# Kernel tuning notes

Hardware: AMD Instinct MI355X
Metric: run time of the kernel (lower is better)

## Reference

```python
import jax, jax.numpy as jnp
import numpy as np

D_MODEL = 1024
N_HEADS = 16
D_K = D_MODEL // N_HEADS
B, S = 4, 2048


def setup_inputs() -> dict:
    key = jax.random.key(0)
    ks = jax.random.split(key, 11)
    scale = 1.0 / np.sqrt(D_MODEL)
    inp = {
        "q": jax.random.normal(ks[0], (B, S, D_MODEL), dtype=jnp.float32),
        "k": jax.random.normal(ks[1], (B, S, D_MODEL), dtype=jnp.float32),
        "v": jax.random.normal(ks[2], (B, S, D_MODEL), dtype=jnp.float32),
        "Wq": jax.random.normal(ks[3], (D_MODEL, D_MODEL), dtype=jnp.float32) * scale,
        "bq": jnp.zeros((D_MODEL,), dtype=jnp.float32),
        "Wk": jax.random.normal(ks[4], (D_MODEL, D_MODEL), dtype=jnp.float32) * scale,
        "bk": jnp.zeros((D_MODEL,), dtype=jnp.float32),
        "Wv": jax.random.normal(ks[5], (D_MODEL, D_MODEL), dtype=jnp.float32) * scale,
        "bv": jnp.zeros((D_MODEL,), dtype=jnp.float32),
        "Wo": jax.random.normal(ks[6], (D_MODEL, D_MODEL), dtype=jnp.float32) * scale,
        "bo": jnp.zeros((D_MODEL,), dtype=jnp.float32),
    }
    return inp


def _split_heads(x):
    # [B, S, D] -> [B, H, S, d_k]
    b, s, _ = x.shape
    return x.reshape(b, s, N_HEADS, D_K).transpose(0, 2, 1, 3)


def reference(q, k, v, Wq, bq, Wk, bk, Wv, bv, Wo, bo):
    Q = _split_heads(q @ Wq.T + bq)  # [B, H, S, d_k]
    K = _split_heads(k @ Wk.T + bk)
    V = _split_heads(v @ Wv.T + bv)
    scale = 1.0 / jnp.sqrt(jnp.asarray(D_K, Q.dtype))
    scores = jnp.einsum("bhqd,bhkd->bhqk", Q, K) * scale  # [B, H, S, S]
    attn = jax.nn.softmax(scores, axis=-1)
    out = jnp.einsum("bhqk,bhkd->bhqd", attn, V)  # [B, H, S, d_k]
    out = out.transpose(0, 2, 1, 3).reshape(q.shape[0], q.shape[1], D_MODEL)
    return out @ Wo.T + bo
```

## Files before the change

### kernel.cpp

```cpp
#include <hip/hip_runtime.h>


typedef __bf16 bf16;
typedef bf16 bf16x4 __attribute__((ext_vector_type(4)));
typedef bf16 bf16x8 __attribute__((ext_vector_type(8)));
typedef float f32x4 __attribute__((ext_vector_type(4)));

__device__ __forceinline__ void gld_lds16(const void* g, void* l) {
  __builtin_amdgcn_global_load_lds((__attribute__((address_space(1))) void*)g,
                                   (__attribute__((address_space(3))) void*)l,
                                   16, 0, 0);
}

__global__ __launch_bounds__(256) void cvt3(const float* __restrict__ a,
                                            const float* __restrict__ b,
                                            const float* __restrict__ c,
                                            bf16* __restrict__ oa,
                                            bf16* __restrict__ ob,
                                            bf16* __restrict__ oc) {
  const int z = blockIdx.y;
  const float* s = (z == 0) ? a : (z == 1) ? b : c;
  bf16* d = (z == 0) ? oa : (z == 1) ? ob : oc;
  const int i = blockIdx.x * 256 + threadIdx.x;
  float4 f = reinterpret_cast<const float4*>(s)[i];
  bf16x4 o = {(bf16)f.x, (bf16)f.y, (bf16)f.z, (bf16)f.w};
  reinterpret_cast<bf16x4*>(d)[i] = o;
}

__global__ __launch_bounds__(256) void cvt4(const float* __restrict__ a,
                                            const float* __restrict__ b,
                                            const float* __restrict__ c,
                                            const float* __restrict__ dd,
                                            bf16* __restrict__ oa,
                                            bf16* __restrict__ ob,
                                            bf16* __restrict__ oc,
                                            bf16* __restrict__ od) {
  const int z = blockIdx.y;
  const float* s = (z == 0) ? a : (z == 1) ? b : (z == 2) ? c : dd;
  bf16* d = (z == 0) ? oa : (z == 1) ? ob : (z == 2) ? oc : od;
  const int i = blockIdx.x * 256 + threadIdx.x;
  float4 f = reinterpret_cast<const float4*>(s)[i];
  bf16x4 o = {(bf16)f.x, (bf16)f.y, (bf16)f.z, (bf16)f.w};
  reinterpret_cast<bf16x4*>(d)[i] = o;
}

__device__ __forceinline__ void gemm_core(const bf16* __restrict__ A,
                                          const bf16* __restrict__ B,
                                          bf16* As, bf16* Bs, int t,
                                          int m0, int n0, f32x4 acc[4][4]) {
  constexpr int K = 1024;
  const int lane = t & 63;
  const int wave = t >> 6;
  const int wm = wave >> 1, wn = wave & 1;
  const int r16 = lane & 15, quad = lane >> 4;

  for (int k0 = 0; k0 < K; k0 += 32) {
    __syncthreads();
#pragma unroll
    for (int hh = 0; hh < 2; ++hh) {
      const int c = t + hh * 256;
      const int row = c >> 2, kk = (c & 3) * 8;
      gld_lds16(A + (size_t)(m0 + row) * K + k0 + kk, As + c * 8);
      gld_lds16(B + (size_t)(n0 + row) * K + k0 + kk, Bs + c * 8);
    }
    __syncthreads();
    bf16x8 af[4], bfr[4];
#pragma unroll
    for (int i = 0; i < 4; ++i)
      af[i] = *(const bf16x8*)&As[(wm * 64 + i * 16 + r16) * 32 + quad * 8];
#pragma unroll
    for (int i = 0; i < 4; ++i)
      bfr[i] = *(const bf16x8*)&Bs[(wn * 64 + i * 16 + r16) * 32 + quad * 8];
#pragma unroll
    for (int mi = 0; mi < 4; ++mi)
#pragma unroll
      for (int ni = 0; ni < 4; ++ni)
        acc[mi][ni] = __builtin_amdgcn_mfma_f32_16x16x32_bf16(af[mi], bfr[ni],
                                                              acc[mi][ni], 0, 0, 0);
  }
}

__global__ __launch_bounds__(256) void gemm_qkv(
    const bf16* __restrict__ qb, const bf16* __restrict__ kb,
    const bf16* __restrict__ vb, const bf16* __restrict__ Wqb,
    const bf16* __restrict__ Wkb, const bf16* __restrict__ Wvb,
    const float* __restrict__ bq, const float* __restrict__ bk,
    const float* __restrict__ bv, bf16* __restrict__ Qp,
    bf16* __restrict__ Kp, bf16* __restrict__ VTt, float qscale) {
  __shared__ alignas(16) bf16 As[128 * 32];
  __shared__ alignas(16) bf16 Bs[128 * 32];
  const int which = blockIdx.z;
  const bf16* A = (which == 0) ? qb : (which == 1) ? kb : vb;
  const bf16* W = (which == 0) ? Wqb : (which == 1) ? Wkb : Wvb;
  const float* bias = (which == 0) ? bq : (which == 1) ? bk : bv;
  const float oscale = (which == 0) ? qscale : 1.0f;
  bf16* Cb = (which == 0) ? Qp : (which == 1) ? Kp : VTt;

  const int t = threadIdx.x;
  const int m0 = blockIdx.y * 128, n0 = blockIdx.x * 128;
  f32x4 acc[4][4] = {};
  gemm_core(A, W, As, Bs, t, m0, n0, acc);

  const int lane = t & 63, wave = t >> 6;
  const int wm = wave >> 1, wn = wave & 1;
  const int r16 = lane & 15, quad = lane >> 4;
#pragma unroll
  for (int mi = 0; mi < 4; ++mi) {
    const int m = m0 + wm * 64 + mi * 16 + quad * 4;
#pragma unroll
    for (int ni = 0; ni < 4; ++ni) {
      const int n = n0 + wn * 64 + ni * 16 + r16;
      const float bv_ = bias[n];
      const int h = n >> 6, dh = n & 63;
      if (which < 2) {
#pragma unroll
        for (int i = 0; i < 4; ++i) {
          const int mm = m + i;
          const int b = mm >> 11, s = mm & 2047;
          Cb[(((size_t)(b * 16 + h)) * 2048 + s) * 64 + dh] =
              (bf16)((acc[mi][ni][i] + bv_) * oscale);
        }
      } else {
        const int b = m >> 11, s = m & 2047;
        bf16x4 pk;
#pragma unroll
        for (int i = 0; i < 4; ++i) pk[i] = (bf16)(acc[mi][ni][i] + bv_);
        *(bf16x4*)&Cb[(((size_t)(b * 16 + h)) * 64 + dh) * 2048 + s] = pk;
      }
    }
  }
}

__global__ __launch_bounds__(256) void gemm_out(const bf16* __restrict__ A,
                                                const bf16* __restrict__ W,
                                                const float* __restrict__ bias,
                                                float* __restrict__ Cf) {
  __shared__ alignas(16) bf16 As[128 * 32];
  __shared__ alignas(16) bf16 Bs[128 * 32];
  const int t = threadIdx.x;
  const int m0 = blockIdx.y * 128, n0 = blockIdx.x * 128;
  f32x4 acc[4][4] = {};
  gemm_core(A, W, As, Bs, t, m0, n0, acc);

  const int lane = t & 63, wave = t >> 6;
  const int wm = wave >> 1, wn = wave & 1;
  const int r16 = lane & 15, quad = lane >> 4;
#pragma unroll
  for (int mi = 0; mi < 4; ++mi) {
    const int m = m0 + wm * 64 + mi * 16 + quad * 4;
#pragma unroll
    for (int ni = 0; ni < 4; ++ni) {
      const int n = n0 + wn * 64 + ni * 16 + r16;
      const float bv_ = bias[n];
#pragma unroll
      for (int i = 0; i < 4; ++i)
        Cf[(size_t)(m + i) * 1024 + n] = acc[mi][ni][i] + bv_;
    }
  }
}

__global__ __launch_bounds__(256) void attn_fwd(const bf16* __restrict__ Qp,
                                                const bf16* __restrict__ Kp,
                                                const bf16* __restrict__ VT,
                                                bf16* __restrict__ AO) {
  __shared__ alignas(16) bf16 Ks[64 * 72];
  __shared__ alignas(16) bf16 Vs[64 * 72];
  __shared__ alignas(16) bf16 Ps[128 * 72];
  __shared__ float Lr[128];
  const int t = threadIdx.x, lane = t & 63, wave = t >> 6;
  const int r16 = lane & 15, quad = lane >> 4;
  const int bh = blockIdx.y;
  const int q0 = blockIdx.x * 128;
  const int qw = wave * 32;
  const bf16* Qb = Qp + (size_t)bh * (2048 * 64);
  const bf16* Kb = Kp + (size_t)bh * (2048 * 64);
  const bf16* Vb = VT + (size_t)bh * (64 * 2048);

  bf16x8 qf[2][2];
#pragma unroll
  for (int nq = 0; nq < 2; ++nq)
#pragma unroll
    for (int ks = 0; ks < 2; ++ks)
      qf[nq][ks] = *(const bf16x8*)&Qb[(size_t)(q0 + qw + nq * 16 + r16) * 64 +
                                       ks * 32 + quad * 8];

  const int c0 = t * 2, c1 = t * 2 + 1;
  const int kr0 = c0 >> 3, kc0 = (c0 & 7) * 8;
  const int kr1 = c1 >> 3, kc1 = (c1 & 7) * 8;

  bf16x8 kreg0 = *(const bf16x8*)(Kb + (size_t)kr0 * 64 + kc0);
  bf16x8 kreg1 = *(const bf16x8*)(Kb + (size_t)kr1 * 64 + kc1);
  bf16x8 vreg0 = *(const bf16x8*)(Vb + (size_t)kr0 * 2048 + kc0);
  bf16x8 vreg1 = *(const bf16x8*)(Vb + (size_t)kr1 * 2048 + kc1);

  f32x4 o[2][4] = {};
  float lrow[2] = {0.f, 0.f};

  for (int kv0 = 0; kv0 < 2048; kv0 += 64) {
    __syncthreads();
    *(bf16x8*)&Ks[kr0 * 72 + kc0] = kreg0;
    *(bf16x8*)&Ks[kr1 * 72 + kc1] = kreg1;
    *(bf16x8*)&Vs[kr0 * 72 + kc0] = vreg0;
    *(bf16x8*)&Vs[kr1 * 72 + kc1] = vreg1;
    __syncthreads();

    if (kv0 + 64 < 2048) {
      const int nx = kv0 + 64;
      kreg0 = *(const bf16x8*)(Kb + (size_t)(nx + kr0) * 64 + kc0);
      kreg1 = *(const bf16x8*)(Kb + (size_t)(nx + kr1) * 64 + kc1);
      vreg0 = *(const bf16x8*)(Vb + (size_t)kr0 * 2048 + nx + kc0);
      vreg1 = *(const bf16x8*)(Vb + (size_t)kr1 * 2048 + nx + kc1);
    }

    bf16x8 kf[4][2];
#pragma unroll
    for (int mi = 0; mi < 4; ++mi) {
      kf[mi][0] = *(const bf16x8*)&Ks[(mi * 16 + r16) * 72 + quad * 8];
      kf[mi][1] = *(const bf16x8*)&Ks[(mi * 16 + r16) * 72 + 32 + quad * 8];
    }

#pragma unroll
    for (int nq = 0; nq < 2; ++nq) {
      const int qL = qw + nq * 16 + r16;
#pragma unroll
      for (int mi = 0; mi < 4; ++mi) {
        f32x4 z = {};
        z = __builtin_amdgcn_mfma_f32_16x16x32_bf16(kf[mi][0], qf[nq][0], z, 0, 0, 0);
        z = __builtin_amdgcn_mfma_f32_16x16x32_bf16(kf[mi][1], qf[nq][1], z, 0, 0, 0);
        bf16x4 pk;
#pragma unroll
        for (int i = 0; i < 4; ++i) {
          const float p = __builtin_amdgcn_exp2f(z[i]);
          lrow[nq] += p;
          pk[i] = (bf16)p;
        }
        *(bf16x4*)&Ps[qL * 72 + mi * 16 + quad * 4] = pk;
      }
    }

#pragma unroll
    for (int ks = 0; ks < 2; ++ks) {
      bf16x8 pf[2];
#pragma unroll
      for (int mi = 0; mi < 2; ++mi)
        pf[mi] = *(const bf16x8*)&Ps[(qw + mi * 16 + r16) * 72 + ks * 32 + quad * 8];
#pragma unroll
      for (int ni = 0; ni < 4; ++ni) {
        bf16x8 vf = *(const bf16x8*)&Vs[(ni * 16 + r16) * 72 + ks * 32 + quad * 8];
#pragma unroll
        for (int mi = 0; mi < 2; ++mi)
          o[mi][ni] = __builtin_amdgcn_mfma_f32_16x16x32_bf16(pf[mi], vf, o[mi][ni], 0, 0, 0);
      }
    }
  }

#pragma unroll
  for (int nq = 0; nq < 2; ++nq) {
    float s = lrow[nq];
    s += __shfl_xor(s, 16);
    s += __shfl_xor(s, 32);
    if (quad == 0) Lr[qw + nq * 16 + r16] = s;
  }
  f32x4 lr[2];
#pragma unroll
  for (int mi = 0; mi < 2; ++mi)
    lr[mi] = *(const f32x4*)&Lr[qw + mi * 16 + quad * 4];

  const int b = bh >> 4, h = bh & 15;
#pragma unroll
  for (int mi = 0; mi < 2; ++mi)
#pragma unroll
    for (int i = 0; i < 4; ++i) {
      const float rl = 1.0f / lr[mi][i];
      const int sq = q0 + qw + mi * 16 + quad * 4 + i;
      const size_t base = ((size_t)(b * 2048 + sq)) * 1024 + h * 64;
#pragma unroll
      for (int ni = 0; ni < 4; ++ni)
        AO[base + ni * 16 + r16] = (bf16)(o[mi][ni][i] * rl);
    }
}

extern "C" void kernel_launch(void* const* d_in, const int* in_sizes, int n_in,
                              void* d_out, int out_size, void* d_ws, size_t ws_size,
                              hipStream_t stream) {
  const float* q  = (const float*)d_in[0];
  const float* k  = (const float*)d_in[1];
  const float* v  = (const float*)d_in[2];
  const float* Wq = (const float*)d_in[3];
  const float* bq = (const float*)d_in[4];
  const float* Wk = (const float*)d_in[5];
  const float* bk = (const float*)d_in[6];
  const float* Wv = (const float*)d_in[7];
  const float* bv = (const float*)d_in[8];
  const float* Wo = (const float*)d_in[9];
  const float* bo = (const float*)d_in[10];

  char* ws = (char*)d_ws;
  const size_t MB = 1ull << 20;
  bf16* qb  = (bf16*)(ws + 0);
  bf16* kb  = (bf16*)(ws + 16 * MB);
  bf16* vb  = (bf16*)(ws + 32 * MB);
  bf16* Wqb = (bf16*)(ws + 48 * MB);
  bf16* Wkb = (bf16*)(ws + 50 * MB);
  bf16* Wvb = (bf16*)(ws + 52 * MB);
  bf16* Wob = (bf16*)(ws + 54 * MB);
  bf16* Qp  = (bf16*)(ws + 56 * MB);
  bf16* Kp  = (bf16*)(ws + 72 * MB);
  bf16* VTt = (bf16*)(ws + 88 * MB);
  bf16* AO  = qb;

  cvt3<<<dim3(8192, 3), 256, 0, stream>>>(q, k, v, qb, kb, vb);
  cvt4<<<dim3(1024, 4), 256, 0, stream>>>(Wq, Wk, Wv, Wo, Wqb, Wkb, Wvb, Wob);

  const float qscale = 0.125f * 1.44269504088896340736f;
  gemm_qkv<<<dim3(8, 64, 3), 256, 0, stream>>>(qb, kb, vb, Wqb, Wkb, Wvb,
                                               bq, bk, bv, Qp, Kp, VTt, qscale);

  attn_fwd<<<dim3(16, 64), 256, 0, stream>>>(Qp, Kp, VTt, AO);

  gemm_out<<<dim3(8, 64), 256, 0, stream>>>(AO, Wob, bo, (float*)d_out);
}
```

Measured before the change: 350.6 us.

## Keep attention probabilities in registers via lane shuffles instead of LDS round-trip

The attention kernel no longer writes the exp'd score tile to a shared-memory P buffer and reads it back. Each wave now rearranges its packed bf16 probabilities into the MFMA A-operand layout with cross-lane shuffles. This drops the Ps LDS array, which lowers shared-memory use and lets launch bounds request 4 blocks per CU. The block index is also remapped to a swizzled order so neighbouring blocks share K/V heads for cache locality. The shuffles add VALU/permute work per tile and may raise register pressure under the tighter occupancy bound.

Measured after the change: 385.7 us. 1.1x slower.

```diff
diff --git a/kernel.cpp b/kernel.cpp
--- a/kernel.cpp
+++ b/kernel.cpp
@@ -5,6 +5,8 @@
 typedef bf16 bf16x4 __attribute__((ext_vector_type(4)));
 typedef bf16 bf16x8 __attribute__((ext_vector_type(8)));
 typedef float f32x4 __attribute__((ext_vector_type(4)));
+typedef int i32x2 __attribute__((ext_vector_type(2)));
+typedef int i32x4 __attribute__((ext_vector_type(4)));
 
 __device__ __forceinline__ void gld_lds16(const void* g, void* l) {
   __builtin_amdgcn_global_load_lds((__attribute__((address_space(1))) void*)g,
@@ -159,18 +161,21 @@
   }
 }
 
-__global__ __launch_bounds__(256) void attn_fwd(const bf16* __restrict__ Qp,
-                                                const bf16* __restrict__ Kp,
-                                                const bf16* __restrict__ VT,
-                                                bf16* __restrict__ AO) {
+__global__ __launch_bounds__(256, 4) void attn_fwd(const bf16* __restrict__ Qp,
+                                                   const bf16* __restrict__ Kp,
+                                                   const bf16* __restrict__ VT,
+                                                   bf16* __restrict__ AO) {
   __shared__ alignas(16) bf16 Ks[64 * 72];
   __shared__ alignas(16) bf16 Vs[64 * 72];
-  __shared__ alignas(16) bf16 Ps[128 * 72];
   __shared__ float Lr[128];
   const int t = threadIdx.x, lane = t & 63, wave = t >> 6;
   const int r16 = lane & 15, quad = lane >> 4;
-  const int bh = blockIdx.y;
-  const int q0 = blockIdx.x * 128;
+
+  const int lin = blockIdx.x + (blockIdx.y << 4);
+  const int w = ((lin & 7) << 7) + (lin >> 3);
+  const int bh = w >> 4;
+  const int q0 = (w & 15) << 7;
+
   const int qw = wave * 32;
   const bf16* Qb = Qp + (size_t)bh * (2048 * 64);
   const bf16* Kb = Kp + (size_t)bh * (2048 * 64);
@@ -192,6 +197,10 @@
   bf16x8 kreg1 = *(const bf16x8*)(Kb + (size_t)kr1 * 64 + kc1);
   bf16x8 vreg0 = *(const bf16x8*)(Vb + (size_t)kr0 * 2048 + kc0);
   bf16x8 vreg1 = *(const bf16x8*)(Vb + (size_t)kr1 * 2048 + kc1);
+
+  const int srcLo = r16 + ((quad & 1) << 5);
+  const int srcHi = srcLo + 16;
+  const bool hiH = (quad & 2) != 0;
 
   f32x4 o[2][4] = {};
   float lrow[2] = {0.f, 0.f};
@@ -219,9 +228,10 @@
       kf[mi][1] = *(const bf16x8*)&Ks[(mi * 16 + r16) * 72 + 32 + quad * 8];
     }
 
+    bf16x8 pfr[2][2];
 #pragma unroll
     for (int nq = 0; nq < 2; ++nq) {
-      const int qL = qw + nq * 16 + r16;
+      int pk_i[4][2];
 #pragma unroll
       for (int mi = 0; mi < 4; ++mi) {
         f32x4 z = {};
@@ -234,22 +244,35 @@
           lrow[nq] += p;
           pk[i] = (bf16)p;
         }
-        *(bf16x4*)&Ps[qL * 72 + mi * 16 + quad * 4] = pk;
+        const i32x2 pp = __builtin_bit_cast(i32x2, pk);
+        pk_i[mi][0] = pp[0];
+        pk_i[mi][1] = pp[1];
       }
+#pragma unroll
+      for (int ks = 0; ks < 2; ++ks) {
+        const int a0 = pk_i[2 * ks][0], a1 = pk_i[2 * ks][1];
+        const int b0 = pk_i[2 * ks + 1][0], b1 = pk_i[2 * ks + 1][1];
+        const int la0 = __shfl(a0, srcLo, 64), la1 = __shfl(a1, srcLo, 64);
+        const int lb0 = __shfl(b0, srcLo, 64), lb1 = __shfl(b1, srcLo, 64);
+        const int ha0 = __shfl(a0, srcHi, 64), ha1 = __shfl(a1, srcHi, 64);
+        const int hb0 = __shfl(b0, srcHi, 64), hb1 = __shfl(b1, srcHi, 64);
+        i32x4 f;
+        f[0] = hiH ? lb0 : la0;
+        f[1] = hiH ? lb1 : la1;
+        f[2] = hiH ? hb0 : ha0;
+        f[3] = hiH ? hb1 : ha1;
+        pfr[nq][ks] = __builtin_bit_cast(bf16x8, f);
+      }
     }
 
 #pragma unroll
     for (int ks = 0; ks < 2; ++ks) {
-      bf16x8 pf[2];
-#pragma unroll
-      for (int mi = 0; mi < 2; ++mi)
-        pf[mi] = *(const bf16x8*)&Ps[(qw + mi * 16 + r16) * 72 + ks * 32 + quad * 8];
 #pragma unroll
       for (int ni = 0; ni < 4; ++ni) {
         bf16x8 vf = *(const bf16x8*)&Vs[(ni * 16 + r16) * 72 + ks * 32 + quad * 8];
 #pragma unroll
-        for (int mi = 0; mi < 2; ++mi)
-          o[mi][ni] = __builtin_amdgcn_mfma_f32_16x16x32_bf16(pf[mi], vf, o[mi][ni], 0, 0, 0);
+        for (int nq = 0; nq < 2; ++nq)
+          o[nq][ni] = __builtin_amdgcn_mfma_f32_16x16x32_bf16(pfr[nq][ks], vf, o[nq][ni], 0, 0, 0);
       }
     }
   }
```
